# Kernel tuning notes

Hardware: AMD Instinct MI355X
Metric: run time of the kernel (lower is better)

The kernel has to match this reference:

```python
import jax, jax.numpy as jnp
import numpy as np

N_NODES = 50000
N_EDGES = 800000
D_IN = 128
D_OUT = 128


def setup_inputs() -> dict:
    key = jax.random.key(0)
    k1, k2, k3, k4, k5 = jax.random.split(key, 5)
    feat = jax.random.normal(k1, (N_NODES, D_IN), dtype=jnp.float32)
    W_neigh = jax.random.normal(k2, (D_OUT, D_IN), dtype=jnp.float32) * (1.0 / np.sqrt(D_IN))
    W_self = jax.random.normal(k3, (D_OUT, D_IN), dtype=jnp.float32) * (1.0 / np.sqrt(D_IN))
    b_self = jnp.zeros((D_OUT,), dtype=jnp.float32)
    src = jax.random.randint(k4, (N_EDGES,), 0, N_NODES, dtype=jnp.int32)
    dst = jax.random.randint(k5, (N_EDGES,), 0, N_NODES, dtype=jnp.int32)
    return {"feat": feat, "W_neigh": W_neigh, "W_self": W_self, "b_self": b_self, "src": src, "dst": dst}


def reference(feat, W_neigh, W_self, b_self, src, dst):
    # SAGEConv 'mean' aggregator, feat_drop=0, edge_weight=None.
    n = feat.shape[0]
    msgs = feat[src]  # copy_u gather: [E, D_IN]
    summed = jax.ops.segment_sum(msgs, dst, num_segments=n)  # [N, D_IN]
    deg = jax.ops.segment_sum(jnp.ones_like(dst, dtype=feat.dtype), dst, num_segments=n)
    h_neigh = summed / jnp.maximum(deg, 1.0)[:, None]  # fn.mean (0 for isolated nodes)
    h_neigh = h_neigh @ W_neigh.T  # fc_neigh (no bias)
    rst = feat @ W_self.T + b_self + h_neigh  # fc_self(h_self) + h_neigh
    return rst
```

## Files before the change

kernel.cpp:

```cpp
#include <hip/hip_runtime.h>
#include <cstddef>
#include <cstdint>

#define N_NODES 50000
#define N_EDGES 800000
#define D 128
#define NWG 128
#define EPW (N_EDGES / NWG)
#define NBUCK 196

typedef __attribute__((ext_vector_type(8))) short bf16x8;
typedef __attribute__((ext_vector_type(16))) float f32x16;

__device__ __forceinline__ unsigned short f32_to_bf16_rne(float x) {
    unsigned u = __builtin_bit_cast(unsigned, x);
    unsigned r = (u + 0x7FFFu + ((u >> 16) & 1u)) >> 16;
    return (unsigned short)r;
}
__device__ __forceinline__ float bf16lo_f32(unsigned u) {
    return __builtin_bit_cast(float, u << 16);
}
__device__ __forceinline__ float bf16hi_f32(unsigned u) {
    return __builtin_bit_cast(float, u & 0xFFFF0000u);
}

__launch_bounds__(256)
__global__ void fconv_kernel(const float* __restrict__ feat,
                             unsigned short* __restrict__ featb) {
    const int i = blockIdx.x * 256 + threadIdx.x;
    if (i >= N_NODES * D / 8) return;
    const float* gp = feat + (size_t)i * 8;
    const float4 a = *(const float4*)gp;
    const float4 b = *(const float4*)(gp + 4);
    bf16x8 h;
    h[0] = (short)f32_to_bf16_rne(a.x); h[1] = (short)f32_to_bf16_rne(a.y);
    h[2] = (short)f32_to_bf16_rne(a.z); h[3] = (short)f32_to_bf16_rne(a.w);
    h[4] = (short)f32_to_bf16_rne(b.x); h[5] = (short)f32_to_bf16_rne(b.y);
    h[6] = (short)f32_to_bf16_rne(b.z); h[7] = (short)f32_to_bf16_rne(b.w);
    *(bf16x8*)&featb[(size_t)i * 8] = h;
}

__launch_bounds__(256)
__global__ void s1_hist_kernel(const int* __restrict__ dst, int* __restrict__ ghist) {
    __shared__ int hist[256];
    const int t = threadIdx.x;
    const int w = blockIdx.x;
    hist[t] = 0;
    __syncthreads();
    const int base = w * EPW;
    for (int i = t; i < EPW; i += 256)
        atomicAdd(&hist[dst[base + i] >> 8], 1);
    __syncthreads();
    ghist[w * 256 + t] = hist[t];
}

__launch_bounds__(256)
__global__ void s2_scan_kernel(const int* __restrict__ ghist,
                               int* __restrict__ gpos,
                               int* __restrict__ gboff) {
    __shared__ int s[256];
    const int b = threadIdx.x;
    int tot = 0;
    for (int w = 0; w < NWG; ++w) tot += ghist[w * 256 + b];
    s[b] = tot;
    __syncthreads();
    for (int d = 1; d < 256; d <<= 1) {
        int v = 0;
        if (b >= d) v = s[b - d];
        __syncthreads();
        s[b] += v;
        __syncthreads();
    }
    const int boff = s[b] - tot;
    gboff[b] = boff;
    if (b == 255) gboff[256] = s[255];
    int run = boff;
    for (int w = 0; w < NWG; ++w) {
        gpos[w * 256 + b] = run;
        run += ghist[w * 256 + b];
    }
}

__launch_bounds__(256)
__global__ void s3_bin_kernel(const int* __restrict__ src,
                              const int* __restrict__ dst,
                              const int* __restrict__ gpos,
                              unsigned* __restrict__ binned) {
    __shared__ int cur[256];
    const int t = threadIdx.x;
    const int w = blockIdx.x;
    cur[t] = gpos[w * 256 + t];
    __syncthreads();
    const int base = w * EPW;
    for (int i = t; i < EPW; i += 256) {
        const int s = src[base + i];
        const int d = dst[base + i];
        const int p = atomicAdd(&cur[d >> 8], 1);
        binned[p] = (unsigned)s | ((unsigned)(d & 255) << 16);
    }
}

__launch_bounds__(256)
__global__ void finalize_kernel(const unsigned* __restrict__ binned,
                                const int* __restrict__ gboff,
                                int* __restrict__ deg_i,
                                int* __restrict__ off,
                                unsigned short* __restrict__ csr_src) {
    __shared__ int c0[256];
    __shared__ int s[256];
    __shared__ int cur[256];
    const int t = threadIdx.x;
    const int b = blockIdx.x;
    c0[t] = 0;
    __syncthreads();
    const int lo = gboff[b], hi = gboff[b + 1];
    for (int i = lo + t; i < hi; i += 256)
        atomicAdd(&c0[(binned[i] >> 16) & 255u], 1);
    __syncthreads();
    const int c = c0[t];
    s[t] = c;
    __syncthreads();
    for (int d = 1; d < 256; d <<= 1) {
        int v = 0;
        if (t >= d) v = s[t - d];
        __syncthreads();
        s[t] += v;
        __syncthreads();
    }
    const int o = gboff[b] + s[t] - c;
    const int node = b * 256 + t;
    if (node < N_NODES) {
        deg_i[node] = c;
        off[node] = o;
    }
    cur[t] = o;
    __syncthreads();
    for (int i = lo + t; i < hi; i += 256) {
        const unsigned u = binned[i];
        const int p = atomicAdd(&cur[(u >> 16) & 255u], 1);
        csr_src[p] = (unsigned short)(u & 0xFFFFu);
    }
}

__launch_bounds__(256)
__global__ void gather_kernel(const unsigned short* __restrict__ featb,
                              const int* __restrict__ off,
                              const int* __restrict__ deg_i,
                              const unsigned short* __restrict__ csr_src,
                              unsigned short* __restrict__ hneighb) {
    const int t = threadIdx.x;
    const int lane8 = (t & 15) * 8;
    const int node = blockIdx.x * 16 + (t >> 4);
    if (node >= N_NODES) return;
    const int s0 = off[node];
    const int cnt = deg_i[node];
    float a0 = 0.f, a1 = 0.f, a2 = 0.f, a3 = 0.f;
    float a4 = 0.f, a5 = 0.f, a6 = 0.f, a7 = 0.f;
    int e = s0;
    const int e4 = s0 + (cnt & ~3);
#define ACC(u) { a0 += bf16lo_f32((u).x); a1 += bf16hi_f32((u).x); \
                 a2 += bf16lo_f32((u).y); a3 += bf16hi_f32((u).y); \
                 a4 += bf16lo_f32((u).z); a5 += bf16hi_f32((u).z); \
                 a6 += bf16lo_f32((u).w); a7 += bf16hi_f32((u).w); }
    for (; e < e4; e += 4) {
        const int i0 = csr_src[e];
        const int i1 = csr_src[e + 1];
        const int i2 = csr_src[e + 2];
        const int i3 = csr_src[e + 3];
        const uint4 u0 = *(const uint4*)&featb[(size_t)i0 * D + lane8];
        const uint4 u1 = *(const uint4*)&featb[(size_t)i1 * D + lane8];
        const uint4 u2 = *(const uint4*)&featb[(size_t)i2 * D + lane8];
        const uint4 u3 = *(const uint4*)&featb[(size_t)i3 * D + lane8];
        ACC(u0); ACC(u1); ACC(u2); ACC(u3);
    }
    for (; e < s0 + cnt; ++e) {
        const uint4 u = *(const uint4*)&featb[(size_t)csr_src[e] * D + lane8];
        ACC(u);
    }
#undef ACC
    const float sc = 1.f / fmaxf((float)cnt, 1.f);
    const unsigned h0 = f32_to_bf16_rne(a0 * sc);
    const unsigned h1 = f32_to_bf16_rne(a1 * sc);
    const unsigned h2 = f32_to_bf16_rne(a2 * sc);
    const unsigned h3 = f32_to_bf16_rne(a3 * sc);
    const unsigned h4 = f32_to_bf16_rne(a4 * sc);
    const unsigned h5 = f32_to_bf16_rne(a5 * sc);
    const unsigned h6 = f32_to_bf16_rne(a6 * sc);
    const unsigned h7 = f32_to_bf16_rne(a7 * sc);
    uint4 o;
    o.x = (h1 << 16) | h0;
    o.y = (h3 << 16) | h2;
    o.z = (h5 << 16) | h4;
    o.w = (h7 << 16) | h6;
    *(uint4*)&hneighb[(size_t)node * D + lane8] = o;
}

__global__ void wsplit_kernel(const float* __restrict__ Wself,
                              const float* __restrict__ Wneigh,
                              unsigned short* __restrict__ Wf) {
    const int unit = blockIdx.x * 256 + threadIdx.x;
    if (unit >= 4096) return;
    const int phase = unit >> 11;
    const int kbi   = (unit >> 9) & 3;
    const int u     = unit & 511;
    const int j     = u & 127;
    const int c     = u >> 7;
    const float* __restrict__ W = phase ? Wneigh : Wself;
    const float* gp = &W[(size_t)j * D + kbi * 32 + c * 8];
    const int p = j >> 5, ks = c >> 1, g = c & 1;
    const size_t base = (size_t)(phase * 4 + kbi) * 4096
                      + (size_t)(((p * 2 + ks) * 64) + (j & 31) + 32 * g) * 8;
#pragma unroll
    for (int e = 0; e < 8; ++e)
        Wf[base + e] = f32_to_bf16_rne(gp[e]);
}

__launch_bounds__(256)
__global__ void gemm_kernel(const unsigned short* __restrict__ featb,
                            const unsigned short* __restrict__ hneighb,
                            const unsigned short* __restrict__ Wf,
                            const float* __restrict__ bias,
                            float* __restrict__ out) {
    __shared__ __align__(16) unsigned short sA[4096];
    __shared__ __align__(16) unsigned short sW[4096];

    const int tid  = threadIdx.x;
    const int wv   = tid >> 6;
    const int l    = tid & 63;
    const int row0 = blockIdx.x * 128;

    f32x16 acc[4] = {};

#pragma unroll 1
    for (int blk = 0; blk < 8; ++blk) {
        const int kbi = blk & 3;
        const unsigned short* __restrict__ A = (blk < 4) ? featb : hneighb;

        __syncthreads();

        {
            const size_t gbase = (size_t)blk * 4096;
#pragma unroll
            for (int i = 0; i < 2; ++i) {
                const int o = (i * 256 + tid) * 8;
                *(bf16x8*)&sW[o] = *(const bf16x8*)&Wf[gbase + o];
            }
        }
#pragma unroll
        for (int i = 0; i < 2; ++i) {
            const int u   = i * 256 + tid;
            const int row = u & 127;
            const int c   = u >> 7;
            const int grow = row0 + row;
            bf16x8 v = {};
            if (grow < N_NODES)
                v = *(const bf16x8*)&A[(size_t)grow * D + kbi * 32 + c * 8];
            const int p = row >> 5, ks = c >> 1, g = c & 1;
            const int o = ((p * 2 + ks) * 64 + (row & 31) + 32 * g) * 8;
            *(bf16x8*)&sA[o] = v;
        }
        __syncthreads();

#pragma unroll
        for (int ks = 0; ks < 2; ++ks) {
            const bf16x8 a = *(const bf16x8*)&sA[((wv * 2 + ks) * 64 + l) * 8];
#pragma unroll
            for (int n = 0; n < 4; ++n) {
                const bf16x8 w = *(const bf16x8*)&sW[((n * 2 + ks) * 64 + l) * 8];
                acc[n] = __builtin_amdgcn_mfma_f32_32x32x16_bf16(a, w, acc[n], 0, 0, 0);
            }
        }
    }

    const int col = l & 31;
    const int hi2 = l >> 5;
    float bv[4];
#pragma unroll
    for (int n = 0; n < 4; ++n) bv[n] = bias[n * 32 + col];
#pragma unroll
    for (int r = 0; r < 16; ++r) {
        const int rloc = (r & 3) + 8 * (r >> 2) + 4 * hi2;
        const int grow = row0 + wv * 32 + rloc;
        if (grow < N_NODES) {
#pragma unroll
            for (int n = 0; n < 4; ++n)
                out[(size_t)grow * D + n * 32 + col] = acc[n][r] + bv[n];
        }
    }
}

extern "C" void kernel_launch(void* const* d_in, const int* in_sizes, int n_in,
                              void* d_out, int out_size, void* d_ws, size_t ws_size,
                              hipStream_t stream) {
    const float* feat  = (const float*)d_in[0];
    const float* Wn    = (const float*)d_in[1];
    const float* Wsf   = (const float*)d_in[2];
    const float* bself = (const float*)d_in[3];
    const int*   src   = (const int*)d_in[4];
    const int*   dst   = (const int*)d_in[5];
    float* out = (float*)d_out;

    unsigned short* featb   = (unsigned short*)d_ws;
    unsigned short* hneighb = featb + (size_t)N_NODES * D;
    unsigned* binned = (unsigned*)(hneighb + (size_t)N_NODES * D);
    unsigned short* csr_src = (unsigned short*)(binned + N_EDGES);
    int*   deg_i     = (int*)(csr_src + N_EDGES);
    int*   off       = deg_i + N_NODES;
    int*   ghist     = off + N_NODES;
    int*   gpos      = ghist + NWG * 256;
    int*   gboff     = gpos + NWG * 256;
    unsigned short* Wf = (unsigned short*)(gboff + 260);

    fconv_kernel<<<(N_NODES * D / 8 + 255) / 256, 256, 0, stream>>>(feat, featb);
    s1_hist_kernel<<<NWG, 256, 0, stream>>>(dst, ghist);
    s2_scan_kernel<<<1, 256, 0, stream>>>(ghist, gpos, gboff);
    s3_bin_kernel<<<NWG, 256, 0, stream>>>(src, dst, gpos, binned);
    finalize_kernel<<<NBUCK, 256, 0, stream>>>(binned, gboff, deg_i, off, csr_src);
    wsplit_kernel<<<16, 256, 0, stream>>>(Wsf, Wn, Wf);
    gather_kernel<<<(N_NODES + 15) / 16, 256, 0, stream>>>(featb, off, deg_i, csr_src, hneighb);

    const int gblocks = (N_NODES + 127) / 128;
    gemm_kernel<<<gblocks, 256, 0, stream>>>(featb, hneighb, Wf, bself, out);
}
```

Measured before the change: 96.32 us.

## Fuse prep kernels, fold scan into binning, unroll gather, double-buffer GEMM

Merges the feature conversion, weight split and histogram kernels into one block-partitioned prep launch. The scan is folded into the binning kernel, with each block recomputing its prefix, so the single-block scan launch goes away. The gather loop is unrolled to eight outstanding loads, and the GEMM now loads all weights into LDS once and double-buffers the A tiles. Together these cut launch count, latency exposure and barriers, at the cost of more LDS per GEMM block (about 80KB, lowering occupancy) and redundant scan work in every binning block.

Result: faster. 89.91 us (-6.7%).

```diff
diff --git a/kernel.cpp b/kernel.cpp
--- a/kernel.cpp
+++ b/kernel.cpp
@@ -8,6 +8,8 @@
 #define NWG 128
 #define EPW (N_EDGES / NWG)
 #define NBUCK 196
+#define FCONV_BLKS 3125
+#define WSPLIT_BLKS 16
 
 typedef __attribute__((ext_vector_type(8))) short bf16x8;
 typedef __attribute__((ext_vector_type(16))) float f32x16;
@@ -25,78 +27,94 @@
 }
 
 __launch_bounds__(256)
-__global__ void fconv_kernel(const float* __restrict__ feat,
-                             unsigned short* __restrict__ featb) {
-    const int i = blockIdx.x * 256 + threadIdx.x;
-    if (i >= N_NODES * D / 8) return;
-    const float* gp = feat + (size_t)i * 8;
-    const float4 a = *(const float4*)gp;
-    const float4 b = *(const float4*)(gp + 4);
-    bf16x8 h;
-    h[0] = (short)f32_to_bf16_rne(a.x); h[1] = (short)f32_to_bf16_rne(a.y);
-    h[2] = (short)f32_to_bf16_rne(a.z); h[3] = (short)f32_to_bf16_rne(a.w);
-    h[4] = (short)f32_to_bf16_rne(b.x); h[5] = (short)f32_to_bf16_rne(b.y);
-    h[6] = (short)f32_to_bf16_rne(b.z); h[7] = (short)f32_to_bf16_rne(b.w);
-    *(bf16x8*)&featb[(size_t)i * 8] = h;
-}
-
-__launch_bounds__(256)
-__global__ void s1_hist_kernel(const int* __restrict__ dst, int* __restrict__ ghist) {
+__global__ void prep_kernel(const float* __restrict__ feat,
+                            const float* __restrict__ Wself,
+                            const float* __restrict__ Wneigh,
+                            const int* __restrict__ dst,
+                            unsigned short* __restrict__ featb,
+                            unsigned short* __restrict__ Wf,
+                            int* __restrict__ ghist) {
     __shared__ int hist[256];
+    const int bid = blockIdx.x;
     const int t = threadIdx.x;
-    const int w = blockIdx.x;
-    hist[t] = 0;
-    __syncthreads();
-    const int base = w * EPW;
-    for (int i = t; i < EPW; i += 256)
-        atomicAdd(&hist[dst[base + i] >> 8], 1);
-    __syncthreads();
-    ghist[w * 256 + t] = hist[t];
-}
-
-__launch_bounds__(256)
-__global__ void s2_scan_kernel(const int* __restrict__ ghist,
-                               int* __restrict__ gpos,
-                               int* __restrict__ gboff) {
-    __shared__ int s[256];
-    const int b = threadIdx.x;
-    int tot = 0;
-    for (int w = 0; w < NWG; ++w) tot += ghist[w * 256 + b];
-    s[b] = tot;
-    __syncthreads();
-    for (int d = 1; d < 256; d <<= 1) {
-        int v = 0;
-        if (b >= d) v = s[b - d];
-        __syncthreads();
-        s[b] += v;
-        __syncthreads();
-    }
-    const int boff = s[b] - tot;
-    gboff[b] = boff;
-    if (b == 255) gboff[256] = s[255];
-    int run = boff;
-    for (int w = 0; w < NWG; ++w) {
-        gpos[w * 256 + b] = run;
-        run += ghist[w * 256 + b];
+    if (bid < FCONV_BLKS) {
+        const int i = bid * 256 + t;
+        if (i >= N_NODES * D / 8) return;
+        const float* gp = feat + (size_t)i * 8;
+        const float4 a = *(const float4*)gp;
+        const float4 b = *(const float4*)(gp + 4);
+        bf16x8 h;
+        h[0] = (short)f32_to_bf16_rne(a.x); h[1] = (short)f32_to_bf16_rne(a.y);
+        h[2] = (short)f32_to_bf16_rne(a.z); h[3] = (short)f32_to_bf16_rne(a.w);
+        h[4] = (short)f32_to_bf16_rne(b.x); h[5] = (short)f32_to_bf16_rne(b.y);
+        h[6] = (short)f32_to_bf16_rne(b.z); h[7] = (short)f32_to_bf16_rne(b.w);
+        *(bf16x8*)&featb[(size_t)i * 8] = h;
+    } else if (bid < FCONV_BLKS + WSPLIT_BLKS) {
+        const int unit = (bid - FCONV_BLKS) * 256 + t;
+        if (unit >= 4096) return;
+        const int phase = unit >> 11;
+        const int kbi   = (unit >> 9) & 3;
+        const int u     = unit & 511;
+        const int j     = u & 127;
+        const int c     = u >> 7;
+        const float* __restrict__ W = phase ? Wneigh : Wself;
+        const float* gp = &W[(size_t)j * D + kbi * 32 + c * 8];
+        const int p = j >> 5, ks = c >> 1, g = c & 1;
+        const size_t base = (size_t)(phase * 4 + kbi) * 4096
+                          + (size_t)(((p * 2 + ks) * 64) + (j & 31) + 32 * g) * 8;
+#pragma unroll
+        for (int e = 0; e < 8; ++e)
+            Wf[base + e] = f32_to_bf16_rne(gp[e]);
+    } else {
+        const int w = bid - FCONV_BLKS - WSPLIT_BLKS;
+        hist[t] = 0;
+        __syncthreads();
+        const int base = w * EPW;
+        for (int i = t; i < EPW; i += 256)
+            atomicAdd(&hist[dst[base + i] >> 8], 1);
+        __syncthreads();
+        ghist[w * 256 + t] = hist[t];
     }
 }
 
 __launch_bounds__(256)
 __global__ void s3_bin_kernel(const int* __restrict__ src,
                               const int* __restrict__ dst,
-                              const int* __restrict__ gpos,
-                              unsigned* __restrict__ binned) {
+                              const int* __restrict__ ghist,
+                              unsigned* __restrict__ binned,
+                              int* __restrict__ gboff) {
+    __shared__ int s[256];
     __shared__ int cur[256];
     const int t = threadIdx.x;
     const int w = blockIdx.x;
-    cur[t] = gpos[w * 256 + t];
+    int tot = 0, mypre = 0;
+    for (int w2 = 0; w2 < NWG; ++w2) {
+        const int v = ghist[w2 * 256 + t];
+        tot += v;
+        if (w2 < w) mypre += v;
+    }
+    s[t] = tot;
+    __syncthreads();
+    for (int d = 1; d < 256; d <<= 1) {
+        int v = 0;
+        if (t >= d) v = s[t - d];
+        __syncthreads();
+        s[t] += v;
+        __syncthreads();
+    }
+    const int boff = s[t] - tot;
+    if (w == 0) {
+        gboff[t] = boff;
+        if (t == 255) gboff[256] = s[255];
+    }
+    cur[t] = boff + mypre;
     __syncthreads();
     const int base = w * EPW;
     for (int i = t; i < EPW; i += 256) {
-        const int s = src[base + i];
+        const int sv = src[base + i];
         const int d = dst[base + i];
         const int p = atomicAdd(&cur[d >> 8], 1);
-        binned[p] = (unsigned)s | ((unsigned)(d & 255) << 16);
+        binned[p] = (unsigned)sv | ((unsigned)(d & 255) << 16);
     }
 }
 
@@ -154,15 +172,35 @@
     if (node >= N_NODES) return;
     const int s0 = off[node];
     const int cnt = deg_i[node];
+    const int end = s0 + cnt;
     float a0 = 0.f, a1 = 0.f, a2 = 0.f, a3 = 0.f;
     float a4 = 0.f, a5 = 0.f, a6 = 0.f, a7 = 0.f;
     int e = s0;
-    const int e4 = s0 + (cnt & ~3);
 #define ACC(u) { a0 += bf16lo_f32((u).x); a1 += bf16hi_f32((u).x); \
                  a2 += bf16lo_f32((u).y); a3 += bf16hi_f32((u).y); \
                  a4 += bf16lo_f32((u).z); a5 += bf16hi_f32((u).z); \
                  a6 += bf16lo_f32((u).w); a7 += bf16hi_f32((u).w); }
-    for (; e < e4; e += 4) {
+    for (; e + 8 <= end; e += 8) {
+        const int i0 = csr_src[e];
+        const int i1 = csr_src[e + 1];
+        const int i2 = csr_src[e + 2];
+        const int i3 = csr_src[e + 3];
+        const int i4 = csr_src[e + 4];
+        const int i5 = csr_src[e + 5];
+        const int i6 = csr_src[e + 6];
+        const int i7 = csr_src[e + 7];
+        const uint4 u0 = *(const uint4*)&featb[(size_t)i0 * D + lane8];
+        const uint4 u1 = *(const uint4*)&featb[(size_t)i1 * D + lane8];
+        const uint4 u2 = *(const uint4*)&featb[(size_t)i2 * D + lane8];
+        const uint4 u3 = *(const uint4*)&featb[(size_t)i3 * D + lane8];
+        const uint4 u4 = *(const uint4*)&featb[(size_t)i4 * D + lane8];
+        const uint4 u5 = *(const uint4*)&featb[(size_t)i5 * D + lane8];
+        const uint4 u6 = *(const uint4*)&featb[(size_t)i6 * D + lane8];
+        const uint4 u7 = *(const uint4*)&featb[(size_t)i7 * D + lane8];
+        ACC(u0); ACC(u1); ACC(u2); ACC(u3);
+        ACC(u4); ACC(u5); ACC(u6); ACC(u7);
+    }
+    for (; e + 4 <= end; e += 4) {
         const int i0 = csr_src[e];
         const int i1 = csr_src[e + 1];
         const int i2 = csr_src[e + 2];
@@ -173,7 +211,7 @@
         const uint4 u3 = *(const uint4*)&featb[(size_t)i3 * D + lane8];
         ACC(u0); ACC(u1); ACC(u2); ACC(u3);
     }
-    for (; e < s0 + cnt; ++e) {
+    for (; e < end; ++e) {
         const uint4 u = *(const uint4*)&featb[(size_t)csr_src[e] * D + lane8];
         ACC(u);
     }
@@ -195,57 +233,29 @@
     *(uint4*)&hneighb[(size_t)node * D + lane8] = o;
 }
 
-__global__ void wsplit_kernel(const float* __restrict__ Wself,
-                              const float* __restrict__ Wneigh,
-                              unsigned short* __restrict__ Wf) {
-    const int unit = blockIdx.x * 256 + threadIdx.x;
-    if (unit >= 4096) return;
-    const int phase = unit >> 11;
-    const int kbi   = (unit >> 9) & 3;
-    const int u     = unit & 511;
-    const int j     = u & 127;
-    const int c     = u >> 7;
-    const float* __restrict__ W = phase ? Wneigh : Wself;
-    const float* gp = &W[(size_t)j * D + kbi * 32 + c * 8];
-    const int p = j >> 5, ks = c >> 1, g = c & 1;
-    const size_t base = (size_t)(phase * 4 + kbi) * 4096
-                      + (size_t)(((p * 2 + ks) * 64) + (j & 31) + 32 * g) * 8;
-#pragma unroll
-    for (int e = 0; e < 8; ++e)
-        Wf[base + e] = f32_to_bf16_rne(gp[e]);
-}
-
 __launch_bounds__(256)
 __global__ void gemm_kernel(const unsigned short* __restrict__ featb,
                             const unsigned short* __restrict__ hneighb,
                             const unsigned short* __restrict__ Wf,
                             const float* __restrict__ bias,
                             float* __restrict__ out) {
-    __shared__ __align__(16) unsigned short sA[4096];
-    __shared__ __align__(16) unsigned short sW[4096];
+    __shared__ __align__(16) unsigned short sW[32768];
+    __shared__ __align__(16) unsigned short sA[2][4096];
 
     const int tid  = threadIdx.x;
     const int wv   = tid >> 6;
     const int l    = tid & 63;
     const int row0 = blockIdx.x * 128;
 
-    f32x16 acc[4] = {};
-
-#pragma unroll 1
-    for (int blk = 0; blk < 8; ++blk) {
+#pragma unroll
+    for (int i = 0; i < 16; ++i) {
+        const int o = (i * 256 + tid) * 8;
+        *(bf16x8*)&sW[o] = *(const bf16x8*)&Wf[o];
+    }
+
+    auto stageA = [&](int sel, int blk) {
         const int kbi = blk & 3;
         const unsigned short* __restrict__ A = (blk < 4) ? featb : hneighb;
-
-        __syncthreads();
-
-        {
-            const size_t gbase = (size_t)blk * 4096;
-#pragma unroll
-            for (int i = 0; i < 2; ++i) {
-                const int o = (i * 256 + tid) * 8;
-                *(bf16x8*)&sW[o] = *(const bf16x8*)&Wf[gbase + o];
-            }
-        }
 #pragma unroll
         for (int i = 0; i < 2; ++i) {
             const int u   = i * 256 + tid;
@@ -257,19 +267,29 @@
                 v = *(const bf16x8*)&A[(size_t)grow * D + kbi * 32 + c * 8];
             const int p = row >> 5, ks = c >> 1, g = c & 1;
             const int o = ((p * 2 + ks) * 64 + (row & 31) + 32 * g) * 8;
-            *(bf16x8*)&sA[o] = v;
+            *(bf16x8*)&sA[sel][o] = v;
         }
-        __syncthreads();
-
+    };
+
+    f32x16 acc[4] = {};
+
+    stageA(0, 0);
+    __syncthreads();
+#pragma unroll 1
+    for (int blk = 0; blk < 8; ++blk) {
+        const int cur = blk & 1;
+        if (blk < 7) stageA(cur ^ 1, blk + 1);
+        const int wbase = blk * 4096;
 #pragma unroll
         for (int ks = 0; ks < 2; ++ks) {
-            const bf16x8 a = *(const bf16x8*)&sA[((wv * 2 + ks) * 64 + l) * 8];
+            const bf16x8 a = *(const bf16x8*)&sA[cur][((wv * 2 + ks) * 64 + l) * 8];
 #pragma unroll
             for (int n = 0; n < 4; ++n) {
-                const bf16x8 w = *(const bf16x8*)&sW[((n * 2 + ks) * 64 + l) * 8];
+                const bf16x8 w = *(const bf16x8*)&sW[wbase + ((n * 2 + ks) * 64 + l) * 8];
                 acc[n] = __builtin_amdgcn_mfma_f32_32x32x16_bf16(a, w, acc[n], 0, 0, 0);
             }
         }
+        __syncthreads();
     }
 
     const int col = l & 31;
@@ -307,16 +327,13 @@
     int*   deg_i     = (int*)(csr_src + N_EDGES);
     int*   off       = deg_i + N_NODES;
     int*   ghist     = off + N_NODES;
-    int*   gpos      = ghist + NWG * 256;
-    int*   gboff     = gpos + NWG * 256;
-    unsigned short* Wf = (unsigned short*)(gboff + 260);
-
-    fconv_kernel<<<(N_NODES * D / 8 + 255) / 256, 256, 0, stream>>>(feat, featb);
-    s1_hist_kernel<<<NWG, 256, 0, stream>>>(dst, ghist);
-    s2_scan_kernel<<<1, 256, 0, stream>>>(ghist, gpos, gboff);
-    s3_bin_kernel<<<NWG, 256, 0, stream>>>(src, dst, gpos, binned);
+    int*   gboff     = ghist + NWG * 256;
+    unsigned short* Wf = (unsigned short*)(gboff + 320);
+
+    prep_kernel<<<FCONV_BLKS + WSPLIT_BLKS + NWG, 256, 0, stream>>>(
+        feat, Wsf, Wn, dst, featb, Wf, ghist);
+    s3_bin_kernel<<<NWG, 256, 0, stream>>>(src, dst, ghist, binned, gboff);
     finalize_kernel<<<NBUCK, 256, 0, stream>>>(binned, gboff, deg_i, off, csr_src);
-    wsplit_kernel<<<16, 256, 0, stream>>>(Wsf, Wn, Wf);
     gather_kernel<<<(N_NODES + 15) / 16, 256, 0, stream>>>(featb, off, deg_i, csr_src, hneighb);
 
     const int gblocks = (N_NODES + 127) / 128;
```
